# Optimization experiments

Hardware: AMD Instinct MI355X
Metric: run time of the kernel (lower is better)

The kernel has to match this reference:

```python
import jax, jax.numpy as jnp
import numpy as np

TOP_K = 2  # matches init kwarg top_k


def setup_inputs() -> dict:
    key = jax.random.key(0)
    k1, k2, k3, k4 = jax.random.split(key, 4)
    B, S, D, E = 4, 2048, 1024, 8
    x = jax.random.normal(k1, (B, S, D), dtype=jnp.float32)
    w_gate = jax.random.normal(k2, (D, E), dtype=jnp.float32) * 0.02
    w1 = jax.random.normal(k3, (E, D, 4 * D), dtype=jnp.float32) * 0.02
    w2 = jax.random.normal(k4, (E, 4 * D, D), dtype=jnp.float32) * 0.02
    return {"x": x, "w_gate": w_gate, "w1": w1, "w2": w2}


def reference(x, w_gate, w1, w2):
    # x: [B, S, D]; w_gate: [D, E]; w1: [E, D, 4D]; w2: [E, 4D, D]
    B, S, D = x.shape
    E = w1.shape[0]
    xt = x.reshape(-1, D)                      # [T, D], T = B*S
    T = xt.shape[0]

    logits = xt @ w_gate                       # [T, E]
    topk_vals, topk_idx = jax.lax.top_k(logits, TOP_K)  # [T, K]
    gates = jax.nn.softmax(topk_vals, axis=-1)          # [T, K]

    # Combine weights per (token, expert): scatter the top-k gates.
    comb = jnp.zeros((T, E), dtype=x.dtype)
    comb = comb.at[jnp.arange(T)[:, None], topk_idx].add(gates)  # [T, E]

    # Dense per-expert FFN over all tokens, masked by combine weight.
    # (Loop over the small fixed expert count; each iteration is a big GEMM.)
    out = jnp.zeros_like(xt)
    for e in range(E):
        h = jax.nn.relu(xt @ w1[e])            # [T, 4D]
        y = h @ w2[e]                          # [T, D]
        out = out + comb[:, e:e + 1] * y
    return out.reshape(B, S, D)
```

## Files before the change

kernel.cpp:

```cpp
#include <hip/hip_runtime.h>
#include <hip/hip_bf16.h>


#define T_TOK   8192
#define DIM     1024
#define NEXP    8
#define HID     4096

typedef unsigned short ushort_t;
typedef __attribute__((ext_vector_type(8))) short bfrag;
typedef __attribute__((ext_vector_type(4))) float f32x4;

__device__ __forceinline__ ushort_t f2bf(float f) {
    union { float f; unsigned int u; } v; v.f = f;
    unsigned int r = v.u + 0x7FFFu + ((v.u >> 16) & 1u);
    return (ushort_t)(r >> 16);
}

__device__ __forceinline__ void async_load16(const void* g, void* l) {
    __builtin_amdgcn_global_load_lds(
        (const __attribute__((address_space(1))) unsigned int*)g,
        (__attribute__((address_space(3))) unsigned int*)l, 16, 0, 0);
}

__global__ __launch_bounds__(256)
void route_kern(const float* __restrict__ x, const float* __restrict__ wg,
                ushort_t* __restrict__ x_bf, int* __restrict__ topk,
                float* __restrict__ gates, int* __restrict__ counts)
{
    const int w = threadIdx.x >> 6, lane = threadIdx.x & 63;
    const int t = blockIdx.x * 4 + w;
    const float* xr = x + (size_t)t * DIM;
    float acc[8];
#pragma unroll
    for (int e = 0; e < 8; ++e) acc[e] = 0.f;

#pragma unroll
    for (int it = 0; it < 4; ++it) {
        const int j = it * 256 + lane * 4;
        float4 xv = *(const float4*)(xr + j);
        ushort4 xb;
        xb.x = f2bf(xv.x); xb.y = f2bf(xv.y); xb.z = f2bf(xv.z); xb.w = f2bf(xv.w);
        *(ushort4*)(x_bf + (size_t)t * DIM + j) = xb;
        const float xs[4] = {xv.x, xv.y, xv.z, xv.w};
#pragma unroll
        for (int jj = 0; jj < 4; ++jj) {
            float4 g0 = *(const float4*)(wg + (size_t)(j + jj) * 8);
            float4 g1 = *(const float4*)(wg + (size_t)(j + jj) * 8 + 4);
            acc[0] += xs[jj] * g0.x; acc[1] += xs[jj] * g0.y;
            acc[2] += xs[jj] * g0.z; acc[3] += xs[jj] * g0.w;
            acc[4] += xs[jj] * g1.x; acc[5] += xs[jj] * g1.y;
            acc[6] += xs[jj] * g1.z; acc[7] += xs[jj] * g1.w;
        }
    }
#pragma unroll
    for (int d = 1; d < 64; d <<= 1)
#pragma unroll
        for (int e = 0; e < 8; ++e) acc[e] += __shfl_xor(acc[e], d);

    if (lane == 0) {
        int i0 = 0; float v0 = acc[0];
#pragma unroll
        for (int e = 1; e < 8; ++e) if (acc[e] > v0) { v0 = acc[e]; i0 = e; }
        int i1 = -1; float v1 = -1e30f;
#pragma unroll
        for (int e = 0; e < 8; ++e) if (e != i0 && acc[e] > v1) { v1 = acc[e]; i1 = e; }
        float ex = __expf(v1 - v0);
        float inv = 1.f / (1.f + ex);
        topk[t * 2] = i0; topk[t * 2 + 1] = i1;
        gates[t * 2] = inv; gates[t * 2 + 1] = ex * inv;
        atomicAdd(&counts[i0], 1);
        atomicAdd(&counts[i1], 1);
    }
}

__global__ void scan_kern(const int* __restrict__ counts, int* __restrict__ offs,
                          int* __restrict__ cursors)
{
    if (threadIdx.x == 0) {
        int o = 0;
        for (int e = 0; e < NEXP; ++e) { offs[e] = o; cursors[e] = o; o += counts[e]; }
        offs[NEXP] = o;
    }
}

__global__ __launch_bounds__(256)
void scatter_kern(const int* __restrict__ topk, const float* __restrict__ gates,
                  int* __restrict__ cursors, int* __restrict__ tok_c,
                  float* __restrict__ gate_c)
{
    const int t = blockIdx.x * 256 + threadIdx.x;
#pragma unroll
    for (int k = 0; k < 2; ++k) {
        int e = topk[t * 2 + k];
        int pos = atomicAdd(&cursors[e], 1);
        tok_c[pos] = t;
        gate_c[pos] = gates[t * 2 + k];
    }
}

__global__ __launch_bounds__(256)
void transp_kern(const float* __restrict__ in, ushort_t* __restrict__ out, int K, int N)
{
    __shared__ float tile[64][65];
    const int e = blockIdx.z;
    const size_t ibase = (size_t)e * K * N, obase = (size_t)e * N * K;
    const int k0 = blockIdx.y * 64, n0 = blockIdx.x * 64;
    const int tid = threadIdx.x;

    const int r = tid >> 4, c4 = (tid & 15) * 4;
#pragma unroll
    for (int p = 0; p < 4; ++p) {
        int kk = p * 16 + r;
        float4 v = *(const float4*)(in + ibase + (size_t)(k0 + kk) * N + n0 + c4);
        tile[kk][c4] = v.x; tile[kk][c4 + 1] = v.y; tile[kk][c4 + 2] = v.z; tile[kk][c4 + 3] = v.w;
    }
    __syncthreads();
    const int nr = tid >> 6, kc = tid & 63;
#pragma unroll
    for (int p = 0; p < 16; ++p) {
        int nn = p * 4 + nr;
        out[obase + (size_t)(n0 + nn) * K + k0 + kc] = f2bf(tile[kc][nn]);
    }
}

template <int STAGE, int NT, int NBLK>
__global__ __launch_bounds__(512, 1)
void gemm256(const ushort_t* __restrict__ A, const ushort_t* __restrict__ Bt,
             ushort_t* __restrict__ Hout, float* __restrict__ Out,
             const int* __restrict__ eoff, const int* __restrict__ tok_c,
             const float* __restrict__ gate_c)
{
    constexpr int K = NT * 64;
    constexpr int N = NBLK * 256;
    constexpr int MB = 32;
    __shared__ ushort_t lds[2][2][256 * 64];

    const int nb = NEXP * MB * NBLK;
    const int orig = blockIdx.x;
    const int lg = (orig & 7) * (nb >> 3) + (orig >> 3);
    const int e = lg / (MB * NBLK);
    const int rem = lg - e * (MB * NBLK);
    const int mblk = rem / NBLK;
    const int nblk = rem - mblk * NBLK;

    const int base = eoff[e];
    const int cnt = eoff[e + 1] - base;
    const int m0 = mblk * 256;
    if (m0 >= cnt) return;
    const int n0 = nblk * 256;

    const int tid = threadIdx.x;
    const int w = tid >> 6, lane = tid & 63;
    const int lhi = lane >> 4, llo = lane & 15;
    const int wm = (w >> 2) << 7;
    const int wn = (w & 3) << 6;

    const ushort_t* Bbase = Bt + (size_t)e * (size_t)N * (size_t)K;
    const ushort_t* asrc[4];
    const ushort_t* bsrc[4];
    int lbase[4];
#pragma unroll
    for (int i = 0; i < 4; ++i) {
        int ci = i * 512 + tid;
        int r = ci >> 3;
        int sb = ((ci & 7) << 4) ^ ((r & 7) << 4);
        int gr = m0 + r; if (gr >= cnt) gr = cnt - 1;
        size_t arow = (STAGE == 1) ? (size_t)tok_c[base + gr] * (size_t)K
                                   : (size_t)(base + gr) * (size_t)K;
        asrc[i] = A + arow + (sb >> 1);
        bsrc[i] = Bbase + (size_t)(n0 + r) * K + (sb >> 1);
        lbase[i] = (i * 8 + w) << 10;
    }

    f32x4 acc[8][4];
#pragma unroll
    for (int m = 0; m < 8; ++m)
#pragma unroll
        for (int n = 0; n < 4; ++n) acc[m][n] = (f32x4)(0.f);

#pragma unroll
    for (int i = 0; i < 4; ++i) {
        async_load16(asrc[i], (char*)lds[0][0] + lbase[i]);
        async_load16(bsrc[i], (char*)lds[0][1] + lbase[i]);
    }
    __syncthreads();

    int cur = 0;
    for (int t = 0; t < NT; ++t) {
        if (t + 1 < NT) {
            const int k0 = (t + 1) << 6;
#pragma unroll
            for (int i = 0; i < 4; ++i) {
                async_load16(asrc[i] + k0, (char*)lds[cur ^ 1][0] + lbase[i]);
                async_load16(bsrc[i] + k0, (char*)lds[cur ^ 1][1] + lbase[i]);
            }
        }
        const char* pA = (const char*)lds[cur][0];
        const char* pB = (const char*)lds[cur][1];
#pragma unroll
        for (int ks = 0; ks < 2; ++ks) {
            const int kb = (ks << 6) + (lhi << 4);
            bfrag a[8], b[4];
#pragma unroll
            for (int m = 0; m < 8; ++m) {
                int row = wm + (m << 4) + llo;
                a[m] = *(const bfrag*)(pA + row * 128 + (kb ^ ((row & 7) << 4)));
            }
#pragma unroll
            for (int n = 0; n < 4; ++n) {
                int row = wn + (n << 4) + llo;
                b[n] = *(const bfrag*)(pB + row * 128 + (kb ^ ((row & 7) << 4)));
            }
#pragma unroll
            for (int m = 0; m < 8; ++m)
#pragma unroll
                for (int n = 0; n < 4; ++n)
                    acc[m][n] = __builtin_amdgcn_mfma_f32_16x16x32_bf16(a[m], b[n], acc[m][n], 0, 0, 0);
        }
        __syncthreads();
        cur ^= 1;
    }

    if (STAGE == 1) {
#pragma unroll
        for (int m = 0; m < 8; ++m)
#pragma unroll
            for (int i = 0; i < 4; ++i) {
                int row = wm + (m << 4) + (lhi << 2) + i;
                int gr = m0 + row;
                if (gr >= cnt) continue;
                size_t rb = (size_t)(base + gr) * (size_t)N + n0 + wn;
#pragma unroll
                for (int n = 0; n < 4; ++n) {
                    float v = acc[m][n][i];
                    Hout[rb + (n << 4) + llo] = f2bf(v > 0.f ? v : 0.f);
                }
            }
    } else {
#pragma unroll
        for (int m = 0; m < 8; ++m)
#pragma unroll
            for (int i = 0; i < 4; ++i) {
                int row = wm + (m << 4) + (lhi << 2) + i;
                int gr = m0 + row;
                if (gr >= cnt) continue;
                int tok = tok_c[base + gr];
                float g = gate_c[base + gr];
                size_t rb = (size_t)tok * (size_t)N + n0 + wn;
#pragma unroll
                for (int n = 0; n < 4; ++n)
                    atomicAdd(&Out[rb + (n << 4) + llo], g * acc[m][n][i]);
            }
    }
}

extern "C" void kernel_launch(void* const* d_in, const int* in_sizes, int n_in,
                              void* d_out, int out_size, void* d_ws, size_t ws_size,
                              hipStream_t stream)
{
    const float* x  = (const float*)d_in[0];
    const float* wg = (const float*)d_in[1];
    const float* w1 = (const float*)d_in[2];
    const float* w2 = (const float*)d_in[3];
    float* out = (float*)d_out;

    char* ws = (char*)d_ws;
    ushort_t* x_bf = (ushort_t*)(ws + 0);
    ushort_t* w1t  = (ushort_t*)(ws + 16777216);
    ushort_t* w2t  = (ushort_t*)(ws + 83886080);
    ushort_t* h    = (ushort_t*)(ws + 150994944);
    char* ctrl     = ws + 285212672;
    int*   topk    = (int*)(ctrl);
    float* gates   = (float*)(ctrl + 65536);
    int*   tok_c   = (int*)(ctrl + 131072);
    float* gate_c  = (float*)(ctrl + 196608);
    int*   counts  = (int*)(ctrl + 262144);
    int*   offs    = (int*)(ctrl + 262144 + 64);
    int*   cursors = (int*)(ctrl + 262144 + 128);

    hipMemsetAsync(counts, 0, NEXP * sizeof(int), stream);
    hipMemsetAsync(out, 0, (size_t)T_TOK * DIM * sizeof(float), stream);

    route_kern<<<T_TOK / 4, 256, 0, stream>>>(x, wg, x_bf, topk, gates, counts);
    transp_kern<<<dim3(HID / 64, DIM / 64, NEXP), 256, 0, stream>>>(w1, w1t, DIM, HID);
    transp_kern<<<dim3(DIM / 64, HID / 64, NEXP), 256, 0, stream>>>(w2, w2t, HID, DIM);
    scan_kern<<<1, 64, 0, stream>>>(counts, offs, cursors);
    scatter_kern<<<T_TOK / 256, 256, 0, stream>>>(topk, gates, cursors, tok_c, gate_c);

    gemm256<1, 16, 16><<<NEXP * 32 * 16, 512, 0, stream>>>(
        x_bf, w1t, h, nullptr, offs, tok_c, gate_c);
    gemm256<2, 64, 4><<<NEXP * 32 * 4, 512, 0, stream>>>(
        h, w2t, nullptr, out, offs, tok_c, gate_c);
}
```

Baseline: 765.3 us.

## Restructure grouped GEMM mainloop into eight-phase interleaved load/MFMA pipeline

Splits the A and B LDS tiles into half-tiles and rewrites the K loop as eight phases per two K-tiles. Each phase issues one half-tile async global-to-LDS load, reads a quarter of the A fragments from LDS, and runs the MFMAs under raised wave priority, with explicit barriers and vmcnt waits. The goal is to hide global and LDS latency behind matrix math with finer-grained overlap than the previous whole-tile double buffer. The manual waitcnt and barrier choreography is fragile and could race or stall if the counts are wrong.

```diff
diff --git a/kernel.cpp b/kernel.cpp
--- a/kernel.cpp
+++ b/kernel.cpp
@@ -10,6 +10,8 @@
 typedef unsigned short ushort_t;
 typedef __attribute__((ext_vector_type(8))) short bfrag;
 typedef __attribute__((ext_vector_type(4))) float f32x4;
+
+#define FENCE() asm volatile("" ::: "memory")
 
 __device__ __forceinline__ ushort_t f2bf(float f) {
     union { float f; unsigned int u; } v; v.f = f;
@@ -134,7 +136,9 @@
     constexpr int K = NT * 64;
     constexpr int N = NBLK * 256;
     constexpr int MB = 32;
-    __shared__ ushort_t lds[2][2][256 * 64];
+    constexpr int NITER = NT / 2;
+    __shared__ ushort_t Alds[2][2][128 * 64];
+    __shared__ ushort_t Blds[2][2][128 * 64];
 
     const int nb = NEXP * MB * NBLK;
     const int orig = blockIdx.x;
@@ -153,25 +157,26 @@
     const int tid = threadIdx.x;
     const int w = tid >> 6, lane = tid & 63;
     const int lhi = lane >> 4, llo = lane & 15;
-    const int wm = (w >> 2) << 7;
-    const int wn = (w & 3) << 6;
-
+    const int wm2 = w >> 2;
+    const int wn4 = w & 3;
+
+    const int rloc = w * 16 + (lane >> 3);
+    const int srcslot = (lane & 7) ^ (lane >> 3);
     const ushort_t* Bbase = Bt + (size_t)e * (size_t)N * (size_t)K;
-    const ushort_t* asrc[4];
-    const ushort_t* bsrc[4];
-    int lbase[4];
-#pragma unroll
-    for (int i = 0; i < 4; ++i) {
-        int ci = i * 512 + tid;
-        int r = ci >> 3;
-        int sb = ((ci & 7) << 4) ^ ((r & 7) << 4);
-        int gr = m0 + r; if (gr >= cnt) gr = cnt - 1;
-        size_t arow = (STAGE == 1) ? (size_t)tok_c[base + gr] * (size_t)K
-                                   : (size_t)(base + gr) * (size_t)K;
-        asrc[i] = A + arow + (sb >> 1);
-        bsrc[i] = Bbase + (size_t)(n0 + r) * K + (sb >> 1);
-        lbase[i] = (i * 8 + w) << 10;
-    }
+    const ushort_t* aP[2][2];
+    const ushort_t* bP[2][2];
+#pragma unroll
+    for (int h = 0; h < 2; ++h)
+#pragma unroll
+        for (int j = 0; j < 2; ++j) {
+            int r = rloc + j * 8;
+            int gr = m0 + h * 128 + r; if (gr >= cnt) gr = cnt - 1;
+            size_t arow = (STAGE == 1) ? (size_t)tok_c[base + gr] * (size_t)K
+                                       : (size_t)(base + gr) * (size_t)K;
+            aP[h][j] = A + arow + srcslot * 8;
+            bP[h][j] = Bbase + (size_t)(n0 + h * 128 + r) * K + srcslot * 8;
+        }
+    const int stoff = w * 2048;
 
     f32x4 acc[8][4];
 #pragma unroll
@@ -179,58 +184,96 @@
 #pragma unroll
         for (int n = 0; n < 4; ++n) acc[m][n] = (f32x4)(0.f);
 
-#pragma unroll
-    for (int i = 0; i < 4; ++i) {
-        async_load16(asrc[i], (char*)lds[0][0] + lbase[i]);
-        async_load16(bsrc[i], (char*)lds[0][1] + lbase[i]);
-    }
-    __syncthreads();
-
-    int cur = 0;
-    for (int t = 0; t < NT; ++t) {
-        if (t + 1 < NT) {
-            const int k0 = (t + 1) << 6;
-#pragma unroll
-            for (int i = 0; i < 4; ++i) {
-                async_load16(asrc[i] + k0, (char*)lds[cur ^ 1][0] + lbase[i]);
-                async_load16(bsrc[i] + k0, (char*)lds[cur ^ 1][1] + lbase[i]);
+    auto stA = [&](int buf, int h, int kt) {
+        char* d = (char*)(&Alds[buf][h][0]) + stoff;
+        async_load16(aP[h][0] + kt * 64, d);
+        async_load16(aP[h][1] + kt * 64, d + 1024);
+    };
+    auto stB = [&](int buf, int h, int kt) {
+        char* d = (char*)(&Blds[buf][h][0]) + stoff;
+        async_load16(bP[h][0] + kt * 64, d);
+        async_load16(bP[h][1] + kt * 64, d + 1024);
+    };
+
+    bfrag af[2][2], bf[4][2];
+    auto ldA = [&](int buf, int q) {
+        const char* p = (const char*)(&Alds[buf][wm2][0]);
+#pragma unroll
+        for (int mi = 0; mi < 2; ++mi) {
+            int r = (q * 2 + mi) * 16 + llo;
+#pragma unroll
+            for (int ks = 0; ks < 2; ++ks) {
+                int kb = ks * 64 + lhi * 16;
+                af[mi][ks] = *(const bfrag*)(p + r * 128 + (kb ^ ((r & 7) << 4)));
             }
         }
-        const char* pA = (const char*)lds[cur][0];
-        const char* pB = (const char*)lds[cur][1];
-#pragma unroll
-        for (int ks = 0; ks < 2; ++ks) {
-            const int kb = (ks << 6) + (lhi << 4);
-            bfrag a[8], b[4];
-#pragma unroll
-            for (int m = 0; m < 8; ++m) {
-                int row = wm + (m << 4) + llo;
-                a[m] = *(const bfrag*)(pA + row * 128 + (kb ^ ((row & 7) << 4)));
+    };
+    auto ldB = [&](int buf) {
+        const char* p = (const char*)(&Blds[buf][wn4 >> 1][0]);
+#pragma unroll
+        for (int n = 0; n < 4; ++n) {
+            int r = (wn4 & 1) * 64 + n * 16 + llo;
+#pragma unroll
+            for (int ks = 0; ks < 2; ++ks) {
+                int kb = ks * 64 + lhi * 16;
+                bf[n][ks] = *(const bfrag*)(p + r * 128 + (kb ^ ((r & 7) << 4)));
             }
-#pragma unroll
-            for (int n = 0; n < 4; ++n) {
-                int row = wn + (n << 4) + llo;
-                b[n] = *(const bfrag*)(pB + row * 128 + (kb ^ ((row & 7) << 4)));
-            }
-#pragma unroll
-            for (int m = 0; m < 8; ++m)
-#pragma unroll
-                for (int n = 0; n < 4; ++n)
-                    acc[m][n] = __builtin_amdgcn_mfma_f32_16x16x32_bf16(a[m], b[n], acc[m][n], 0, 0, 0);
         }
-        __syncthreads();
-        cur ^= 1;
-    }
+    };
+
+#define PH(q, rb, LOADB, STAGE_STMT, VMW)                          \
+    {                                                              \
+        if (LOADB) ldB(rb);                                        \
+        ldA(rb, q);                                                \
+        STAGE_STMT;                                                \
+        FENCE(); __builtin_amdgcn_s_barrier(); FENCE();            \
+        asm volatile("s_waitcnt lgkmcnt(0)" ::: "memory");         \
+        __builtin_amdgcn_sched_barrier(0);                         \
+        __builtin_amdgcn_s_setprio(1);                             \
+        _Pragma("unroll")                                          \
+        for (int mi = 0; mi < 2; ++mi)                             \
+            _Pragma("unroll")                                      \
+            for (int n = 0; n < 4; ++n)                            \
+                _Pragma("unroll")                                  \
+                for (int ks = 0; ks < 2; ++ks)                     \
+                    acc[(q) * 2 + mi][n] = __builtin_amdgcn_mfma_f32_16x16x32_bf16( \
+                        af[mi][ks], bf[n][ks], acc[(q) * 2 + mi][n], 0, 0, 0);      \
+        __builtin_amdgcn_s_setprio(0);                             \
+        VMW;                                                       \
+        FENCE(); __builtin_amdgcn_s_barrier(); FENCE();            \
+    }
+
+    stA(0, 0, 0); stA(0, 1, 0); stB(0, 0, 0); stB(0, 1, 0);
+    stB(1, 0, 1); stB(1, 1, 1);
+    asm volatile("s_waitcnt vmcnt(0)" ::: "memory");
+    FENCE(); __builtin_amdgcn_s_barrier(); FENCE();
+
+    for (int it = 0; it < NITER; ++it) {
+        const int kt0 = 2 * it, kt1 = 2 * it + 1;
+        const bool nx = (it + 1 < NITER);
+        PH(0, 0, true,  stA(1, 0, kt1), );
+        PH(1, 0, false, stA(1, 1, kt1), );
+        PH(2, 0, false, if (nx) stB(0, 0, kt0 + 2), );
+        PH(3, 0, false, if (nx) stB(0, 1, kt0 + 2),
+           if (nx) { asm volatile("s_waitcnt vmcnt(4)" ::: "memory"); }
+           else    { asm volatile("s_waitcnt vmcnt(0)" ::: "memory"); } );
+        PH(0, 1, true,  if (nx) stA(0, 0, kt0 + 2), );
+        PH(1, 1, false, if (nx) stA(0, 1, kt0 + 2), );
+        PH(2, 1, false, if (nx) stB(1, 0, kt1 + 2), );
+        PH(3, 1, false, if (nx) stB(1, 1, kt1 + 2),
+           asm volatile("s_waitcnt vmcnt(4)" ::: "memory"); );
+    }
+#undef PH
 
     if (STAGE == 1) {
 #pragma unroll
         for (int m = 0; m < 8; ++m)
 #pragma unroll
             for (int i = 0; i < 4; ++i) {
-                int row = wm + (m << 4) + (lhi << 2) + i;
+                int row = wm2 * 128 + (m << 4) + (lhi << 2) + i;
                 int gr = m0 + row;
                 if (gr >= cnt) continue;
-                size_t rb = (size_t)(base + gr) * (size_t)N + n0 + wn;
+                size_t rb = (size_t)(base + gr) * (size_t)N + n0 + wn4 * 64;
 #pragma unroll
                 for (int n = 0; n < 4; ++n) {
                     float v = acc[m][n][i];
@@ -242,12 +285,12 @@
         for (int m = 0; m < 8; ++m)
 #pragma unroll
             for (int i = 0; i < 4; ++i) {
-                int row = wm + (m << 4) + (lhi << 2) + i;
+                int row = wm2 * 128 + (m << 4) + (lhi << 2) + i;
                 int gr = m0 + row;
                 if (gr >= cnt) continue;
                 int tok = tok_c[base + gr];
                 float g = gate_c[base + gr];
-                size_t rb = (size_t)tok * (size_t)N + n0 + wn;
+                size_t rb = (size_t)tok * (size_t)N + n0 + wn4 * 64;
 #pragma unroll
                 for (int n = 0; n < 4; ++n)
                     atomicAdd(&Out[rb + (n << 4) + llo], g * acc[m][n][i]);
```

New measurement: 812.0 us. 6.1% more time.
